# Performance work log

Measured on AMD Instinct MI355X. Metric: run time of the kernel, lower is better.

## Reference

```python
import jax, jax.numpy as jnp
import numpy as np

H, W, T = 720, 1280, 20
B, N = 8, 500000


def setup_inputs() -> dict:
    key = jax.random.key(0)
    kx, ky, kt, kp, kc = jax.random.split(key, 5)
    x = jnp.floor(jax.random.uniform(kx, (B, N)) * W)          # pixel x in [0, W)
    y = jnp.floor(jax.random.uniform(ky, (B, N)) * H)          # pixel y in [0, H)
    t = jax.random.uniform(kt, (B, N))                          # normalized time in [0, 1]
    p = jax.random.bernoulli(kp, 0.5, (B, N)).astype(jnp.float32)  # polarity {0,1}
    eventBlock = jnp.stack([x, y, t, p], axis=-1).astype(jnp.float32)  # (B, N, 4)
    eventCounts = jax.random.randint(kc, (B,), N // 2, N + 1).astype(jnp.int64)
    return {"eventBlock": eventBlock, "eventCounts": eventCounts}


def reference(eventBlock, eventCounts):
    # events -> (B, W, H, T) voxel grid via temporal bilinear scatter-add,
    # then permute(0,3,2,1) -> (B, T, H, W) as in EV2VoxelGrid.forward
    x = eventBlock[..., 0].astype(jnp.int32)                    # (B, N)
    y = eventBlock[..., 1].astype(jnp.int32)
    t = eventBlock[..., 2]
    pol = eventBlock[..., 3] * 2.0 - 1.0                        # {0,1} -> {-1,+1}

    valid = jnp.arange(N)[None, :] < eventCounts[:, None]       # (B, N) mask by counts

    tb = t * (T - 1)                                            # continuous bin coord
    k0 = jnp.floor(tb).astype(jnp.int32)
    w1 = tb - k0.astype(tb.dtype)
    w0 = 1.0 - w1
    k0c = jnp.clip(k0, 0, T - 1)
    k1c = jnp.clip(k0 + 1, 0, T - 1)

    xc = jnp.clip(x, 0, W - 1)
    yc = jnp.clip(y, 0, H - 1)
    b = jnp.arange(B, dtype=jnp.int32)[:, None]                 # (B, 1)
    base = ((b * W + xc) * H + yc) * T                          # flat (b, x, y) offset

    v0 = jnp.where(valid, pol * w0, 0.0)
    v1 = jnp.where(valid, pol * w1, 0.0)

    grid = jnp.zeros((B * W * H * T,), dtype=eventBlock.dtype)
    grid = grid.at[(base + k0c).ravel()].add(v0.ravel())
    grid = grid.at[(base + k1c).ravel()].add(v1.ravel())
    grid = grid.reshape(B, W, H, T)
    return jnp.transpose(grid, (0, 3, 2, 1))                    # (B, T, H, W)
```

## Files before the change

kernel.cpp:

```cpp
#include <hip/hip_runtime.h>

#define GH 720
#define GW 1280
#define GT 20
#define GB 8
#define NEV 500000
#define TOTAL (GB * NEV)

#define CY 90
#define NCOARSE (GB * CY)
#define CAPC 6144
#define PAD 32
#define EVB 8192
#define NBLK1 ((TOTAL + EVB - 1) / EVB)
#define PTHREADS 1024

#define TY 8
#define TX 64
#define NTXB (GW / TX)
#define NFINE (NCOARSE * NTXB)
#define CAPF 512
#define MCHUNK 1024
#define NCH (CAPC / MCHUNK)
#define OVF_CAP (1u << 20)

typedef float vfloat4 __attribute__((ext_vector_type(4)));


__global__ __launch_bounds__(256) void k_zero(unsigned* __restrict__ gcnt,
                                              unsigned* __restrict__ fcnt)
{
    int i = blockIdx.x * blockDim.x + threadIdx.x;
    if (i < NCOARSE * PAD + 1) gcnt[i] = 0u;
    if (i < NFINE) fcnt[i] = 0u;
}

__global__ __launch_bounds__(PTHREADS) void k_part(
    const float4* __restrict__ ev, const int* __restrict__ counts,
    unsigned* __restrict__ gcnt, unsigned* __restrict__ buckets,
    uint2* __restrict__ ovf)
{
    __shared__ unsigned hist[NCOARSE];
    const int tid = threadIdx.x;
    const int base = blockIdx.x * EVB + tid;

    for (int c = tid; c < NCOARSE; c += PTHREADS) hist[c] = 0u;
    __syncthreads();

    for (int j = 0; j < EVB / PTHREADS; j++) {
        int i = base + j * PTHREADS;
        if (i >= TOTAL) break;
        int b = i / NEV;
        int n = i - b * NEV;
        if (n >= counts[b]) continue;
        float4 e = ev[i];
        int y = min(max((int)e.y, 0), GH - 1);
        atomicAdd(&hist[b * CY + (y >> 3)], 1u);
    }
    __syncthreads();

    for (int c = tid; c < NCOARSE; c += PTHREADS) {
        unsigned h = hist[c];
        hist[c] = h ? atomicAdd(&gcnt[c * PAD], h) : 0u;
    }
    __syncthreads();

    for (int j = 0; j < EVB / PTHREADS; j++) {
        int i = base + j * PTHREADS;
        if (i >= TOTAL) break;
        int b = i / NEV;
        int n = i - b * NEV;
        if (n >= counts[b]) continue;
        float4 e = ev[i];
        int x = min(max((int)e.x, 0), GW - 1);
        int y = min(max((int)e.y, 0), GH - 1);
        int c = b * CY + (y >> 3);

        float tb = e.z * (float)(GT - 1);
        int k0 = (int)floorf(tb);
        float w1 = tb - (float)k0;
        int k0c = min(max(k0, 0), GT - 1);
        unsigned p = (e.w > 0.5f) ? 1u : 0u;

        unsigned pos = atomicAdd(&hist[c], 1u);
        if (pos < CAPC) {
            unsigned w1q = __float2uint_rn(w1 * 4095.0f);
            unsigned rec = (unsigned)x | ((unsigned)(y & 7) << 11) | (p << 14)
                         | ((unsigned)k0c << 15) | (w1q << 20);
            buckets[(size_t)c * CAPC + pos] = rec;
        } else {
            unsigned word0 = (unsigned)x | ((unsigned)y << 11) | (p << 21)
                           | ((unsigned)k0c << 22) | ((unsigned)b << 27);
            unsigned o = atomicAdd(&gcnt[NCOARSE * PAD], 1u);
            if (o < OVF_CAP) ovf[o] = make_uint2(word0, __float_as_uint(w1));
        }
    }
}

__global__ __launch_bounds__(256) void k_mid(
    const unsigned* __restrict__ buckets, unsigned* __restrict__ gcnt,
    unsigned* __restrict__ fcnt, unsigned* __restrict__ buckets2,
    uint2* __restrict__ ovf)
{
    __shared__ unsigned stash[MCHUNK];
    __shared__ unsigned fh[NTXB], fbase[NTXB], fh2[NTXB];
    const int c = blockIdx.x / NCH;
    const int chunk = blockIdx.x % NCH;
    const int tid = threadIdx.x;

    unsigned m = min(gcnt[c * PAD], (unsigned)CAPC);
    unsigned lo = chunk * MCHUNK;
    if (lo >= m) return;
    unsigned cnt = min(m - lo, (unsigned)MCHUNK);

    if (tid < NTXB) { fh[tid] = 0u; fh2[tid] = 0u; }
    __syncthreads();

    const unsigned* bp = buckets + (size_t)c * CAPC + lo;
    for (unsigned i = tid; i < cnt; i += 256) {
        unsigned r = bp[i];
        stash[i] = r;
        atomicAdd(&fh[(r & 2047u) >> 6], 1u);
    }
    __syncthreads();

    if (tid < NTXB && fh[tid])
        fbase[tid] = atomicAdd(&fcnt[c * NTXB + tid], fh[tid]);
    __syncthreads();

    for (unsigned i = tid; i < cnt; i += 256) {
        unsigned r = stash[i];
        unsigned tx = (r & 2047u) >> 6;
        unsigned dst = fbase[tx] + atomicAdd(&fh2[tx], 1u);
        if (dst < CAPF) {
            buckets2[(size_t)(c * NTXB + tx) * CAPF + dst] = r;
        } else {
            int b = c / CY;
            int y = (c % CY) * 8 + ((r >> 11) & 7);
            unsigned word0 = (r & 2047u) | ((unsigned)y << 11)
                           | (((r >> 14) & 1u) << 21)
                           | (((r >> 15) & 31u) << 22) | ((unsigned)b << 27);
            float w1 = (float)(r >> 20) * (1.0f / 4095.0f);
            unsigned o = atomicAdd(&gcnt[NCOARSE * PAD], 1u);
            if (o < OVF_CAP) ovf[o] = make_uint2(word0, __float_as_uint(w1));
        }
    }
}

__global__ __launch_bounds__(256) void k_accum(
    const unsigned* __restrict__ buckets2, const unsigned* __restrict__ fcnt,
    float* __restrict__ out)
{
    __shared__ float tile[GT * TY * TX];
    const int f = blockIdx.x;
    const int tid = threadIdx.x;

    vfloat4* t4 = (vfloat4*)tile;
    for (int j = tid; j < GT * TY * (TX / 4); j += 256)
        t4[j] = (vfloat4){0.f, 0.f, 0.f, 0.f};
    __syncthreads();

    unsigned m = min(fcnt[f], (unsigned)CAPF);
    const unsigned* bp = buckets2 + (size_t)f * CAPF;
    for (unsigned idx = tid; idx < m; idx += 256) {
        unsigned r = bp[idx];
        int xx = r & 63;
        int yy = (r >> 11) & 7;
        float pol = ((r >> 14) & 1u) ? 1.0f : -1.0f;
        int k0 = (r >> 15) & 31;
        float w1 = (float)(r >> 20) * (1.0f / 4095.0f);
        int k1 = min(k0 + 1, GT - 1);
        atomicAdd(&tile[(k0 * TY + yy) * TX + xx], pol * (1.0f - w1));
        atomicAdd(&tile[(k1 * TY + yy) * TX + xx], pol * w1);
    }
    __syncthreads();

    const int c  = f / NTXB;
    const int tx = f % NTXB;
    const int b  = c / CY;
    const int y0 = (c % CY) * TY;
    vfloat4* o4 = (vfloat4*)out;
    for (int j = tid; j < GT * TY * (TX / 4); j += 256) {
        int row = j >> 4;
        int col = j & 15;
        int k  = row >> 3;
        int yy = row & 7;
        int off = ((b * GT + k) * GH + (y0 + yy)) * (GW / 4) + tx * (TX / 4) + col;
        __builtin_nontemporal_store(t4[j], &o4[off]);
    }
}

__global__ __launch_bounds__(256) void k_overflow(
    const uint2* __restrict__ ovf, const unsigned* __restrict__ gcnt,
    float* __restrict__ out)
{
    unsigned n = min(gcnt[NCOARSE * PAD], OVF_CAP);
    for (unsigned i = blockIdx.x * blockDim.x + threadIdx.x; i < n;
         i += gridDim.x * blockDim.x) {
        uint2 r = ovf[i];
        int x  = r.x & 2047;
        int y  = (r.x >> 11) & 1023;
        int p  = (r.x >> 21) & 1;
        int k0 = (r.x >> 22) & 31;
        int b  = (r.x >> 27) & 7;
        float w1 = __uint_as_float(r.y);
        float w0 = 1.0f - w1;
        float pol = p ? 1.0f : -1.0f;
        int k1 = min(k0 + 1, GT - 1);
        atomicAdd(&out[((b * GT + k0) * GH + y) * GW + x], pol * w0);
        atomicAdd(&out[((b * GT + k1) * GH + y) * GW + x], pol * w1);
    }
}

__global__ __launch_bounds__(256) void ev2voxel_scatter(
    const float4* __restrict__ ev, const int* __restrict__ counts,
    float* __restrict__ out)
{
    int i = blockIdx.x * blockDim.x + threadIdx.x;
    if (i >= TOTAL) return;
    int b = i / NEV;
    int n = i - b * NEV;
    if (n >= counts[b]) return;
    float4 e = ev[i];
    int x = min(max((int)e.x, 0), GW - 1);
    int y = min(max((int)e.y, 0), GH - 1);
    float pol = e.w * 2.0f - 1.0f;
    float tb = e.z * (float)(GT - 1);
    int k0 = (int)floorf(tb);
    float w1 = tb - (float)k0;
    float w0 = 1.0f - w1;
    int k0c = min(max(k0, 0), GT - 1);
    int k1c = min(max(k0 + 1, 0), GT - 1);
    int rowbase = (b * GT) * GH;
    atomicAdd(&out[(rowbase + k0c * GH + y) * GW + x], pol * w0);
    atomicAdd(&out[(rowbase + k1c * GH + y) * GW + x], pol * w1);
}

extern "C" void kernel_launch(void* const* d_in, const int* in_sizes, int n_in,
                              void* d_out, int out_size, void* d_ws, size_t ws_size,
                              hipStream_t stream) {
    const float4* ev = (const float4*)d_in[0];
    const int* counts = (const int*)d_in[1];
    float* out = (float*)d_out;

    const size_t gcnt_off    = 0;
    const size_t fcnt_off    = (size_t)NCOARSE * PAD + PAD;
    const size_t bucket_off  = fcnt_off + NFINE;
    const size_t bucket2_off = bucket_off + (size_t)NCOARSE * CAPC;
    size_t ovf_off           = bucket2_off + (size_t)NFINE * CAPF;
    if (ovf_off & 1) ovf_off++;
    const size_t need_bytes = (ovf_off + (size_t)OVF_CAP * 2) * 4;

    if (ws_size < need_bytes) {
        (void)hipMemsetAsync(out, 0, (size_t)out_size * sizeof(float), stream);
        ev2voxel_scatter<<<(TOTAL + 255) / 256, 256, 0, stream>>>(ev, counts, out);
        return;
    }

    unsigned* ws = (unsigned*)d_ws;
    unsigned* gcnt     = ws + gcnt_off;
    unsigned* fcnt     = ws + fcnt_off;
    unsigned* buckets  = ws + bucket_off;
    unsigned* buckets2 = ws + bucket2_off;
    uint2*    ovf      = (uint2*)(ws + ovf_off);

    k_zero<<<(NCOARSE * PAD + 1 + 255) / 256, 256, 0, stream>>>(gcnt, fcnt);
    k_part<<<NBLK1, PTHREADS, 0, stream>>>(ev, counts, gcnt, buckets, ovf);
    k_mid<<<NCOARSE * NCH, 256, 0, stream>>>(buckets, gcnt, fcnt, buckets2, ovf);
    k_accum<<<NFINE, 256, 0, stream>>>(buckets2, fcnt, out);
    k_overflow<<<64, 256, 0, stream>>>(ovf, gcnt, out);
}
```

Measured before the change: 164.8 us.

## Stash packed events in shared memory and fold overflow handling into accumulation

The partition kernel now reads each event once, packs its record and bin id into shared memory, and reuses them for the scatter pass instead of rereading global memory. The separate overflow kernel is removed; each accumulation block scans the overflow list and adds only its own tile's entries. This cuts global event traffic and one launch, at the cost of about 50 KB of shared memory per partition block and a full overflow scan per tile whenever overflow occurs.

```diff
diff --git a/kernel.cpp b/kernel.cpp
--- a/kernel.cpp
+++ b/kernel.cpp
@@ -40,6 +40,8 @@
     unsigned* __restrict__ gcnt, unsigned* __restrict__ buckets,
     uint2* __restrict__ ovf)
 {
+    __shared__ unsigned stash[EVB];
+    __shared__ unsigned short binid[EVB];
     __shared__ unsigned hist[NCOARSE];
     const int tid = threadIdx.x;
     const int base = blockIdx.x * EVB + tid;
@@ -49,28 +51,16 @@
 
     for (int j = 0; j < EVB / PTHREADS; j++) {
         int i = base + j * PTHREADS;
-        if (i >= TOTAL) break;
-        int b = i / NEV;
-        int n = i - b * NEV;
-        if (n >= counts[b]) continue;
-        float4 e = ev[i];
-        int y = min(max((int)e.y, 0), GH - 1);
-        atomicAdd(&hist[b * CY + (y >> 3)], 1u);
-    }
-    __syncthreads();
-
-    for (int c = tid; c < NCOARSE; c += PTHREADS) {
-        unsigned h = hist[c];
-        hist[c] = h ? atomicAdd(&gcnt[c * PAD], h) : 0u;
-    }
-    __syncthreads();
-
-    for (int j = 0; j < EVB / PTHREADS; j++) {
-        int i = base + j * PTHREADS;
-        if (i >= TOTAL) break;
-        int b = i / NEV;
-        int n = i - b * NEV;
-        if (n >= counts[b]) continue;
+        int slot = j * PTHREADS + tid;
+        int b = 0, n = 0;
+        bool valid = (i < TOTAL);
+        if (valid) {
+            b = i / NEV;
+            n = i - b * NEV;
+            valid = (n < counts[b]);
+        }
+        if (!valid) { binid[slot] = 0xFFFFu; continue; }
+
         float4 e = ev[i];
         int x = min(max((int)e.x, 0), GW - 1);
         int y = min(max((int)e.y, 0), GH - 1);
@@ -81,16 +71,35 @@
         float w1 = tb - (float)k0;
         int k0c = min(max(k0, 0), GT - 1);
         unsigned p = (e.w > 0.5f) ? 1u : 0u;
-
+        unsigned w1q = __float2uint_rn(w1 * 4095.0f);
+        stash[slot] = (unsigned)x | ((unsigned)(y & 7) << 11) | (p << 14)
+                    | ((unsigned)k0c << 15) | (w1q << 20);
+        binid[slot] = (unsigned short)c;
+        atomicAdd(&hist[c], 1u);
+    }
+    __syncthreads();
+
+    for (int c = tid; c < NCOARSE; c += PTHREADS) {
+        unsigned h = hist[c];
+        hist[c] = h ? atomicAdd(&gcnt[c * PAD], h) : 0u;
+    }
+    __syncthreads();
+
+    for (int j = 0; j < EVB / PTHREADS; j++) {
+        int slot = j * PTHREADS + tid;
+        unsigned c = binid[slot];
+        if (c == 0xFFFFu) continue;
+        unsigned r = stash[slot];
         unsigned pos = atomicAdd(&hist[c], 1u);
         if (pos < CAPC) {
-            unsigned w1q = __float2uint_rn(w1 * 4095.0f);
-            unsigned rec = (unsigned)x | ((unsigned)(y & 7) << 11) | (p << 14)
-                         | ((unsigned)k0c << 15) | (w1q << 20);
-            buckets[(size_t)c * CAPC + pos] = rec;
+            buckets[(size_t)c * CAPC + pos] = r;
         } else {
-            unsigned word0 = (unsigned)x | ((unsigned)y << 11) | (p << 21)
-                           | ((unsigned)k0c << 22) | ((unsigned)b << 27);
+            int b = c / CY;
+            int y = (c % CY) * 8 + ((r >> 11) & 7);
+            unsigned word0 = (r & 2047u) | ((unsigned)y << 11)
+                           | (((r >> 14) & 1u) << 21)
+                           | (((r >> 15) & 31u) << 22) | ((unsigned)b << 27);
+            float w1 = (float)(r >> 20) * (1.0f / 4095.0f);
             unsigned o = atomicAdd(&gcnt[NCOARSE * PAD], 1u);
             if (o < OVF_CAP) ovf[o] = make_uint2(word0, __float_as_uint(w1));
         }
@@ -149,10 +158,13 @@
 
 __global__ __launch_bounds__(256) void k_accum(
     const unsigned* __restrict__ buckets2, const unsigned* __restrict__ fcnt,
+    const unsigned* __restrict__ gcnt, const uint2* __restrict__ ovf,
     float* __restrict__ out)
 {
     __shared__ float tile[GT * TY * TX];
     const int f = blockIdx.x;
+    const int c  = f / NTXB;
+    const int tx = f % NTXB;
     const int tid = threadIdx.x;
 
     vfloat4* t4 = (vfloat4*)tile;
@@ -173,10 +185,26 @@
         atomicAdd(&tile[(k0 * TY + yy) * TX + xx], pol * (1.0f - w1));
         atomicAdd(&tile[(k1 * TY + yy) * TX + xx], pol * w1);
     }
-    __syncthreads();
-
-    const int c  = f / NTXB;
-    const int tx = f % NTXB;
+
+    unsigned novf = min(gcnt[NCOARSE * PAD], OVF_CAP);
+    if (novf) {
+        for (unsigned i = tid; i < novf; i += 256) {
+            uint2 r = ovf[i];
+            int x  = r.x & 2047;
+            int y  = (r.x >> 11) & 1023;
+            int b  = (r.x >> 27) & 7;
+            if (b * CY + (y >> 3) != c || (x >> 6) != tx) continue;
+            int p  = (r.x >> 21) & 1;
+            int k0 = (r.x >> 22) & 31;
+            float w1 = __uint_as_float(r.y);
+            float pol = p ? 1.0f : -1.0f;
+            int k1 = min(k0 + 1, GT - 1);
+            atomicAdd(&tile[(k0 * TY + (y & 7)) * TX + (x & 63)], pol * (1.0f - w1));
+            atomicAdd(&tile[(k1 * TY + (y & 7)) * TX + (x & 63)], pol * w1);
+        }
+    }
+    __syncthreads();
+
     const int b  = c / CY;
     const int y0 = (c % CY) * TY;
     vfloat4* o4 = (vfloat4*)out;
@@ -187,28 +215,6 @@
         int yy = row & 7;
         int off = ((b * GT + k) * GH + (y0 + yy)) * (GW / 4) + tx * (TX / 4) + col;
         __builtin_nontemporal_store(t4[j], &o4[off]);
-    }
-}
-
-__global__ __launch_bounds__(256) void k_overflow(
-    const uint2* __restrict__ ovf, const unsigned* __restrict__ gcnt,
-    float* __restrict__ out)
-{
-    unsigned n = min(gcnt[NCOARSE * PAD], OVF_CAP);
-    for (unsigned i = blockIdx.x * blockDim.x + threadIdx.x; i < n;
-         i += gridDim.x * blockDim.x) {
-        uint2 r = ovf[i];
-        int x  = r.x & 2047;
-        int y  = (r.x >> 11) & 1023;
-        int p  = (r.x >> 21) & 1;
-        int k0 = (r.x >> 22) & 31;
-        int b  = (r.x >> 27) & 7;
-        float w1 = __uint_as_float(r.y);
-        float w0 = 1.0f - w1;
-        float pol = p ? 1.0f : -1.0f;
-        int k1 = min(k0 + 1, GT - 1);
-        atomicAdd(&out[((b * GT + k0) * GH + y) * GW + x], pol * w0);
-        atomicAdd(&out[((b * GT + k1) * GH + y) * GW + x], pol * w1);
     }
 }
 
@@ -267,6 +273,5 @@
     k_zero<<<(NCOARSE * PAD + 1 + 255) / 256, 256, 0, stream>>>(gcnt, fcnt);
     k_part<<<NBLK1, PTHREADS, 0, stream>>>(ev, counts, gcnt, buckets, ovf);
     k_mid<<<NCOARSE * NCH, 256, 0, stream>>>(buckets, gcnt, fcnt, buckets2, ovf);
-    k_accum<<<NFINE, 256, 0, stream>>>(buckets2, fcnt, out);
-    k_overflow<<<64, 256, 0, stream>>>(ovf, gcnt, out);
-}
+    k_accum<<<NFINE, 256, 0, stream>>>(buckets2, fcnt, gcnt, ovf, out);
+}
```

Result: faster. 159.4 us (-3.3%).
